# Performance work log

Hardware: AMD Instinct MI355X
Metric: run time of the kernel (lower is better)

## Reference

```python
import jax, jax.numpy as jnp
import numpy as np

N_NODES = 100000


def _sage_conv(x, src, dst, Wl, Wr, b):
    # PyG SAGEConv (aggr='mean'): out = lin_l(mean_j x_j) + lin_r(x_i)
    deg = jax.ops.segment_sum(jnp.ones_like(src, dtype=x.dtype), dst, num_segments=N_NODES)
    agg = jax.ops.segment_sum(x[src], dst, num_segments=N_NODES)
    agg = agg / jnp.clip(deg, 1.0)[:, None]
    return agg @ Wl.T + x @ Wr.T + b


def setup_inputs() -> dict:
    key = jax.random.key(0)
    ks = jax.random.split(key, 16)
    N, E, ES = N_NODES, 1600000, 100000
    IN, H, D = 64, 128, 64

    def lin(k, out_c, in_c):
        s = 1.0 / np.sqrt(in_c)
        return jax.random.uniform(k, (out_c, in_c), jnp.float32, -s, s)

    inp = {
        "x": jax.random.normal(ks[0], (N, IN), jnp.float32),
        "edge_index": jax.random.randint(ks[1], (2, E), 0, N, jnp.int64),
        "edge_sample": jax.random.randint(ks[2], (2, ES), 0, N, jnp.int64),
        # SAGEConv 0: 64 -> 128
        "Wl0": lin(ks[3], H, IN), "Wr0": lin(ks[4], H, IN), "b0": jnp.zeros((H,), jnp.float32),
        # SAGEConv 1: 128 -> 128
        "Wl1": lin(ks[5], H, H), "Wr1": lin(ks[6], H, H), "b1": jnp.zeros((H,), jnp.float32),
        # SAGEConv 2: 128 -> 64
        "Wl2": lin(ks[7], D, H), "Wr2": lin(ks[8], D, H), "b2": jnp.zeros((D,), jnp.float32),
        # feature decoder MLP: 64 -> 128 -> 64
        "Wd1": lin(ks[9], H, D), "bd1": jnp.zeros((H,), jnp.float32),
        "Wd2": lin(ks[10], IN, H), "bd2": jnp.zeros((IN,), jnp.float32),
    }
    return inp


def reference(x, edge_index, edge_sample, Wl0, Wr0, b0, Wl1, Wr1, b1, Wl2, Wr2, b2, Wd1, bd1, Wd2, bd2):
    src, dst = edge_index[0], edge_index[1]
    # encoder (dropout = identity at inference)
    h = jax.nn.relu(_sage_conv(x, src, dst, Wl0, Wr0, b0))
    h = jax.nn.relu(_sage_conv(h, src, dst, Wl1, Wr1, b1))
    emb = _sage_conv(h, src, dst, Wl2, Wr2, b2)
    # feature decoder
    rec = jax.nn.relu(emb @ Wd1.T + bd1) @ Wd2.T + bd2
    # edge decoder: dot product
    edge_scores = jnp.sum(emb[edge_sample[0]] * emb[edge_sample[1]], axis=1)
    return emb, rec, edge_scores
```

## Files before the change

### kernel.cpp

```cpp
#include <hip/hip_runtime.h>

#define NN 100000
#define NBK 196
#define CHUNK 8192
typedef unsigned int uint;
typedef unsigned short ushort;

using f32x4 = __attribute__((ext_vector_type(4))) float;
using s16x8 = __attribute__((ext_vector_type(8))) short;

__device__ inline ushort f32_to_bf16(float f) {
  uint u = __float_as_uint(f);
  uint r = (u + 0x7FFFu + ((u >> 16) & 1u)) >> 16;
  return (ushort)r;
}
__device__ inline float bf16_to_f32(ushort h) {
  return __uint_as_float(((uint)h) << 16);
}

typedef __attribute__((address_space(1))) const unsigned int gas_u32;
typedef __attribute__((address_space(3))) unsigned int las_u32;
__device__ __forceinline__ void gld_lds16(const void* gp, void* lp) {
  __builtin_amdgcn_global_load_lds((gas_u32*)gp, (las_u32*)lp, 16, 0, 0);
}

struct P8 { const float* p[8]; };

__global__ void k_prep(const int* __restrict__ dst, uint* __restrict__ bcnt,
                       uint* __restrict__ chunkCnt, int E, int NCB,
                       const float* __restrict__ x, ushort* __restrict__ xb, int n4, int NC,
                       P8 w, ushort* __restrict__ whi, int wtotal) {
  int b = blockIdx.x;
  int tid = threadIdx.x;
  if (b < NCB) {
    __shared__ uint hist[NBK];
    for (int i = tid; i < NBK; i += 256) hist[i] = 0;
    __syncthreads();
    int base = b * CHUNK;
    int lim = min(base + CHUNK, E);
    for (int e = base + tid; e < lim; e += 256) atomicAdd(&hist[(uint)dst[e] >> 9], 1u);
    __syncthreads();
    for (int i = tid; i < NBK; i += 256) {
      uint h = hist[i];
      chunkCnt[(i << 8) + b] = h;
      if (h) atomicAdd(&bcnt[i], h);
    }
  } else if (b < NCB + NC) {
    int i = (b - NCB) * 256 + tid;
    if (i < n4) {
      float4 v = ((const float4*)x)[i];
      uint2 o;
      o.x = (uint)f32_to_bf16(v.x) | ((uint)f32_to_bf16(v.y) << 16);
      o.y = (uint)f32_to_bf16(v.z) | ((uint)f32_to_bf16(v.w) << 16);
      ((uint2*)xb)[i] = o;
    }
  } else {
    int g = (b - NCB - NC) * 256 + tid;
    if (g < wtotal) {
      const int offs[8] = {0, 8192, 16384, 32768, 49152, 57344, 65536, 73728};
      int s = 0;
#pragma unroll
      for (int i = 1; i < 8; ++i) s += (g >= offs[i]);
      whi[g] = f32_to_bf16(w.p[s][g - offs[s]]);
    }
  }
}

__global__ void k_bscan(const uint* __restrict__ bcnt, uint* __restrict__ bbase,
                        int* __restrict__ rp, const uint* __restrict__ chunkCnt,
                        uint* __restrict__ chunkBase, int NCB) {
  int bk = blockIdx.x;
  int l = threadIdx.x;
  uint p = 0, tot = 0;
  for (int i = l; i < NBK; i += 64) {
    uint v = bcnt[i];
    tot += v;
    if (i < bk) p += v;
  }
#pragma unroll
  for (int off = 1; off < 64; off <<= 1) {
    p += __shfl_xor(p, off, 64);
    tot += __shfl_xor(tot, off, 64);
  }
  if (l == 0) {
    bbase[bk] = p;
    if (bk == 0) { bbase[NBK] = tot; rp[NN] = (int)tot; }
  }
  uint carry = p;
#pragma unroll
  for (int seg = 0; seg < 4; ++seg) {
    int c = seg * 64 + l;
    uint v = (c < NCB) ? chunkCnt[(bk << 8) + c] : 0u;
    uint incl = v;
#pragma unroll
    for (int off = 1; off < 64; off <<= 1) {
      uint t = __shfl_up(incl, off, 64);
      if (l >= off) incl += t;
    }
    if (c < NCB) chunkBase[(bk << 8) + c] = carry + incl - v;
    carry += __shfl(incl, 63, 64);
  }
}

__global__ void k_bscatter(const int* __restrict__ src, const int* __restrict__ dst,
                           const uint* __restrict__ chunkBase, uint* __restrict__ packed, int E) {
  __shared__ uint cur[NBK];
  int tid = threadIdx.x;
  int b = blockIdx.x;
  for (int i = tid; i < NBK; i += 256) cur[i] = chunkBase[(i << 8) + b];
  __syncthreads();
  int base = b * CHUNK;
  int lim = min(base + CHUNK, E);
  for (int e = base + tid; e < lim; e += 256) {
    uint d = (uint)dst[e];
    uint s = (uint)src[e];
    uint bk = d >> 9;
    uint p = atomicAdd(&cur[bk], 1u);
    packed[p] = ((d & 511u) << 20) | s;
  }
}

__global__ void k_build(const uint* __restrict__ bbase, const uint* __restrict__ packed,
                        int* __restrict__ rp, int* __restrict__ col) {
  __shared__ uint hist[512];
  __shared__ uint ws[256];
  int b = blockIdx.x;
  int tid = threadIdx.x;
  uint lo = bbase[b], hi = bbase[b + 1];
  hist[tid] = 0;
  hist[tid + 256] = 0;
  __syncthreads();
  for (uint e = lo + tid; e < hi; e += 256) atomicAdd(&hist[packed[e] >> 20], 1u);
  __syncthreads();
  uint v0 = hist[tid * 2], v1 = hist[tid * 2 + 1];
  ws[tid] = v0 + v1;
  __syncthreads();
  for (int off = 1; off < 256; off <<= 1) {
    uint add = (tid >= off) ? ws[tid - off] : 0u;
    __syncthreads();
    ws[tid] += add;
    __syncthreads();
  }
  uint ex = (tid > 0) ? ws[tid - 1] : 0u;
  hist[tid * 2] = ex;
  hist[tid * 2 + 1] = ex + v0;
  int nodeBase = b << 9;
#pragma unroll
  for (int i = 0; i < 2; ++i) {
    int node = nodeBase + tid * 2 + i;
    if (node < NN) rp[node] = (int)(lo + hist[tid * 2 + i]);
  }
  __syncthreads();
  for (uint e = lo + tid; e < hi; e += 256) {
    uint pk = packed[e];
    uint p = atomicAdd(&hist[pk >> 20], 1u);
    col[lo + p] = (int)(pk & 0xFFFFFu);
  }
}

#define ACC1(vv) { alo += __uint_as_float((vv) << 16); ahi += __uint_as_float((vv) & 0xffff0000u); }

template <int F, int MODE>
__global__ void k_agg(const ushort* __restrict__ x, const int* __restrict__ rp,
                      const int* __restrict__ col, const ushort* __restrict__ u,
                      float* __restrict__ of, ushort* __restrict__ ob, int n) {
  constexpr int RS = F / 2;
  int wave = (blockIdx.x * blockDim.x + threadIdx.x) >> 6;
  int lane = threadIdx.x & 63;
  int node, l;
  if (F == 128) { node = wave; l = lane; }
  else { node = wave * 2 + (lane >> 5); l = lane & 31; }
  if (node >= n) return;
  int beg = rp[node], end = rp[node + 1];
  int deg = end - beg;
  const uint* __restrict__ xu = (const uint*)x;
  float alo = 0.f, ahi = 0.f;
  int j = beg;
  for (; j + 8 <= end; j += 8) {
    int c0 = col[j], c1 = col[j + 1], c2 = col[j + 2], c3 = col[j + 3];
    int c4 = col[j + 4], c5 = col[j + 5], c6 = col[j + 6], c7 = col[j + 7];
    uint v0 = xu[(size_t)c0 * RS + l];
    uint v1 = xu[(size_t)c1 * RS + l];
    uint v2 = xu[(size_t)c2 * RS + l];
    uint v3 = xu[(size_t)c3 * RS + l];
    uint v4 = xu[(size_t)c4 * RS + l];
    uint v5 = xu[(size_t)c5 * RS + l];
    uint v6 = xu[(size_t)c6 * RS + l];
    uint v7 = xu[(size_t)c7 * RS + l];
    ACC1(v0) ACC1(v1) ACC1(v2) ACC1(v3) ACC1(v4) ACC1(v5) ACC1(v6) ACC1(v7)
  }
  if (j + 4 <= end) {
    int c0 = col[j], c1 = col[j + 1], c2 = col[j + 2], c3 = col[j + 3];
    uint v0 = xu[(size_t)c0 * RS + l];
    uint v1 = xu[(size_t)c1 * RS + l];
    uint v2 = xu[(size_t)c2 * RS + l];
    uint v3 = xu[(size_t)c3 * RS + l];
    ACC1(v0) ACC1(v1) ACC1(v2) ACC1(v3)
    j += 4;
  }
  for (; j < end; ++j) {
    uint v0 = xu[(size_t)col[j] * RS + l];
    ACC1(v0)
  }
  float inv = 1.0f / (float)(deg > 0 ? deg : 1);
  alo *= inv;
  ahi *= inv;
  if (MODE == 0) {
    ((uint*)ob)[(size_t)node * RS + l] = (uint)f32_to_bf16(alo) | ((uint)f32_to_bf16(ahi) << 16);
  } else {
    uint uv = ((const uint*)u)[(size_t)node * RS + l];
    float e0 = alo + __uint_as_float(uv << 16);
    float e1 = ahi + __uint_as_float(uv & 0xffff0000u);
    ((float2*)of)[(size_t)node * RS + l] = make_float2(e0, e1);
    ((uint*)ob)[(size_t)node * RS + l] = (uint)f32_to_bf16(e0) | ((uint)f32_to_bf16(e1) << 16);
  }
}

template <int K, bool RELU, bool DUAL, int OUTM>
__global__ __launch_bounds__(256) void k_gemm(
    const ushort* __restrict__ A, const ushort* __restrict__ Wa,
    const ushort* __restrict__ B, const ushort* __restrict__ Wb,
    const float* __restrict__ bias,
    ushort* __restrict__ outu, ushort* __restrict__ outb, int n) {
  constexpr int BM = 64;
  constexpr int KT = 32;
  constexpr int TPP = K / KT;
  constexpr int T = (DUAL ? 2 : 1) * TPP;
  __shared__ ushort As[2][BM * KT];
  __shared__ ushort Ws[2][128 * KT];

  const int tid = threadIdx.x;
  const int lane = tid & 63;
  const int wid = tid >> 6;
  const int fr = lane & 15;
  const int fq = lane >> 4;
  const int blockRow = blockIdx.x * BM;
  const int rowBase = (wid >> 1) * 32;
  const int colBase = (wid & 1) * 64;
  const int srow = lane >> 2;
  const int sksrc = (lane & 3) ^ ((lane >> 3) & 3);
  const bool fullTile = (blockRow + BM <= n);

  f32x4 acc[2][4];
#pragma unroll
  for (int mi = 0; mi < 2; ++mi)
#pragma unroll
    for (int ni = 0; ni < 4; ++ni) acc[mi][ni] = (f32x4){0.f, 0.f, 0.f, 0.f};

  auto stage = [&](int buf, int t) {
    const ushort* __restrict__ Ap = (DUAL && t >= TPP) ? B : A;
    const ushort* __restrict__ Wp = (DUAL && t >= TPP) ? Wb : Wa;
    const int ktb = (t % TPP) * KT;
    {
      int r0 = wid * 16;
      gld_lds16(Ap + (size_t)(blockRow + r0 + srow) * K + ktb + sksrc * 8,
                (char*)As[buf] + r0 * 64);
    }
#pragma unroll
    for (int i = 0; i < 2; ++i) {
      int r0 = (wid + i * 4) * 16;
      gld_lds16(Wp + (size_t)(r0 + srow) * K + ktb + sksrc * 8,
                (char*)Ws[buf] + r0 * 64);
    }
  };
  auto compute = [&](int buf) {
    s16x8 af[2], wf[4];
#pragma unroll
    for (int mi = 0; mi < 2; ++mi) {
      int r = rowBase + mi * 16 + fr;
      af[mi] = *(const s16x8*)((const char*)As[buf] + r * 64 + ((fq ^ ((r >> 1) & 3)) << 4));
    }
#pragma unroll
    for (int ni = 0; ni < 4; ++ni) {
      int r = colBase + ni * 16 + fr;
      wf[ni] = *(const s16x8*)((const char*)Ws[buf] + r * 64 + ((fq ^ ((r >> 1) & 3)) << 4));
    }
#pragma unroll
    for (int mi = 0; mi < 2; ++mi)
#pragma unroll
      for (int ni = 0; ni < 4; ++ni)
        acc[mi][ni] = __builtin_amdgcn_mfma_f32_16x16x32_bf16(af[mi], wf[ni], acc[mi][ni], 0, 0, 0);
  };

  if (fullTile) {
    stage(0, 0);
#pragma unroll
    for (int t = 0; t < T; ++t) {
      if (t + 1 < T) {
        stage((t + 1) & 1, t + 1);
        asm volatile("s_waitcnt vmcnt(3)" ::: "memory");
      } else {
        asm volatile("s_waitcnt vmcnt(0)" ::: "memory");
      }
      __builtin_amdgcn_sched_barrier(0);
      __builtin_amdgcn_s_barrier();
      compute(t & 1);
      if (t + 1 < T) __builtin_amdgcn_s_barrier();
    }
  } else {
#pragma unroll
    for (int t = 0; t < T; ++t) {
      const ushort* __restrict__ Ap = (DUAL && t >= TPP) ? B : A;
      const ushort* __restrict__ Wp = (DUAL && t >= TPP) ? Wb : Wa;
      const int ktb = (t % TPP) * KT;
      __syncthreads();
      {
        int c = tid;
        int r = c >> 2, s = c & 3;
        int row = blockRow + r;
        int ds = s ^ ((r >> 1) & 3);
        uint4 v = make_uint4(0u, 0u, 0u, 0u);
        if (row < n) v = *(const uint4*)(Ap + (size_t)row * K + ktb + s * 8);
        *(uint4*)((char*)As[0] + r * 64 + (ds << 4)) = v;
      }
      for (int c = tid; c < 128 * 4; c += 256) {
        int r = c >> 2, s = c & 3;
        int ds = s ^ ((r >> 1) & 3);
        *(uint4*)((char*)Ws[0] + r * 64 + (ds << 4)) =
            *(const uint4*)(Wp + (size_t)r * K + ktb + s * 8);
      }
      __syncthreads();
      compute(0);
    }
  }

#pragma unroll
  for (int mi = 0; mi < 2; ++mi) {
#pragma unroll
    for (int ni = 0; ni < 4; ++ni) {
#pragma unroll
      for (int r = 0; r < 4; ++r) {
        int row = blockRow + rowBase + mi * 16 + fq * 4 + r;
        int colI = colBase + ni * 16 + fr;
        if (row < n) {
          float v = acc[mi][ni][r];
          if (OUTM == 3) {
            if (colI < 64)
              outb[(size_t)row * 64 + colI] = f32_to_bf16(v);
            else
              outu[(size_t)row * 64 + (colI - 64)] = f32_to_bf16(v + bias[colI - 64]);
          } else {
            if (bias) v += bias[colI];
            if (RELU) v = fmaxf(v, 0.f);
            outb[(size_t)row * 128 + colI] = f32_to_bf16(v);
          }
        }
      }
    }
  }
}

__global__ __launch_bounds__(256) void k_dec(
    const ushort* __restrict__ emb, const ushort* __restrict__ Wd1,
    const float* __restrict__ bd1, const ushort* __restrict__ Wd2,
    const float* __restrict__ bd2, float* __restrict__ rec, int n) {
  __shared__ ushort smem[24 * 1024];
  ushort* As = smem;
  ushort* W1 = smem + 8192;
  ushort* W2 = smem + 16384;
  ushort* Hs = smem;

  const int tid = threadIdx.x;
  const int lane = tid & 63;
  const int wid = tid >> 6;
  const int fr = lane & 15;
  const int fq = lane >> 4;
  const int blockRow = blockIdx.x * 128;
  const int rowBase1 = (wid >> 1) * 64;
  const int colBase1 = (wid & 1) * 64;
  const int srow8 = lane >> 3, sl8 = lane & 7;
  const int srow4 = lane >> 4, sl16 = lane & 15;
  const bool fullTile = (blockRow + 128 <= n);

  if (fullTile) {
#pragma unroll
    for (int i = 0; i < 4; ++i) {
      int r0 = (wid + i * 4) * 8;
      gld_lds16(emb + (size_t)(blockRow + r0 + srow8) * 64 + (sl8 ^ srow8) * 8,
                (char*)As + r0 * 128);
    }
#pragma unroll
    for (int i = 0; i < 4; ++i) {
      int r0 = (wid + i * 4) * 8;
      gld_lds16(Wd1 + (size_t)(r0 + srow8) * 64 + (sl8 ^ srow8) * 8, (char*)W1 + r0 * 128);
    }
#pragma unroll
    for (int i = 0; i < 4; ++i) {
      int r0 = (wid + i * 4) * 4;
      int grow = r0 + srow4;
      gld_lds16(Wd2 + (size_t)grow * 128 + (sl16 ^ (grow & 7)) * 8, (char*)W2 + r0 * 256);
    }
  } else {
    for (int c = tid; c < 128 * 8; c += 256) {
      int r = c >> 3, s = c & 7;
      int row = blockRow + r;
      uint4 v = make_uint4(0u, 0u, 0u, 0u);
      if (row < n) v = *(const uint4*)(emb + (size_t)row * 64 + s * 8);
      *(uint4*)((char*)As + r * 128 + ((s ^ (r & 7)) << 4)) = v;
    }
    for (int c = tid; c < 128 * 8; c += 256) {
      int r = c >> 3, s = c & 7;
      *(uint4*)((char*)W1 + r * 128 + ((s ^ (r & 7)) << 4)) =
          *(const uint4*)(Wd1 + (size_t)r * 64 + s * 8);
    }
    for (int c = tid; c < 64 * 16; c += 256) {
      int r = c >> 4, s = c & 15;
      *(uint4*)((char*)W2 + r * 256 + ((s ^ (r & 7)) << 4)) =
          *(const uint4*)(Wd2 + (size_t)r * 128 + s * 8);
    }
  }
  __syncthreads();

  f32x4 a1[4][4];
#pragma unroll
  for (int mi = 0; mi < 4; ++mi)
#pragma unroll
    for (int ni = 0; ni < 4; ++ni) a1[mi][ni] = (f32x4){0.f, 0.f, 0.f, 0.f};
#pragma unroll
  for (int ks = 0; ks < 2; ++ks) {
    s16x8 af[4], wf[4];
#pragma unroll
    for (int mi = 0; mi < 4; ++mi) {
      int r = rowBase1 + mi * 16 + fr;
      af[mi] = *(const s16x8*)((const char*)As + r * 128 + (((ks * 4 + fq) ^ (r & 7)) << 4));
    }
#pragma unroll
    for (int ni = 0; ni < 4; ++ni) {
      int r = colBase1 + ni * 16 + fr;
      wf[ni] = *(const s16x8*)((const char*)W1 + r * 128 + (((ks * 4 + fq) ^ (r & 7)) << 4));
    }
#pragma unroll
    for (int mi = 0; mi < 4; ++mi)
#pragma unroll
      for (int ni = 0; ni < 4; ++ni)
        a1[mi][ni] = __builtin_amdgcn_mfma_f32_16x16x32_bf16(af[mi], wf[ni], a1[mi][ni], 0, 0, 0);
  }
  __syncthreads();
#pragma unroll
  for (int mi = 0; mi < 4; ++mi) {
#pragma unroll
    for (int ni = 0; ni < 4; ++ni) {
#pragma unroll
      for (int r = 0; r < 4; ++r) {
        int rowl = rowBase1 + mi * 16 + fq * 4 + r;
        int colI = colBase1 + ni * 16 + fr;
        float v = fmaxf(a1[mi][ni][r] + bd1[colI], 0.f);
        int byte = rowl * 256 + ((((colI >> 3) ^ (rowl & 7))) << 4) + (colI & 7) * 2;
        *(ushort*)((char*)Hs + byte) = f32_to_bf16(v);
      }
    }
  }
  __syncthreads();

  f32x4 a2[2][4];
#pragma unroll
  for (int mi = 0; mi < 2; ++mi)
#pragma unroll
    for (int ni = 0; ni < 4; ++ni) a2[mi][ni] = (f32x4){0.f, 0.f, 0.f, 0.f};
#pragma unroll
  for (int kk = 0; kk < 4; ++kk) {
    s16x8 af[2], wf[4];
#pragma unroll
    for (int mi = 0; mi < 2; ++mi) {
      int r = wid * 32 + mi * 16 + fr;
      af[mi] = *(const s16x8*)((const char*)Hs + r * 256 + (((kk * 4 + fq) ^ (r & 7)) << 4));
    }
#pragma unroll
    for (int ni = 0; ni < 4; ++ni) {
      int r = ni * 16 + fr;
      wf[ni] = *(const s16x8*)((const char*)W2 + r * 256 + (((kk * 4 + fq) ^ (r & 7)) << 4));
    }
#pragma unroll
    for (int mi = 0; mi < 2; ++mi)
#pragma unroll
      for (int ni = 0; ni < 4; ++ni)
        a2[mi][ni] = __builtin_amdgcn_mfma_f32_16x16x32_bf16(af[mi], wf[ni], a2[mi][ni], 0, 0, 0);
  }
#pragma unroll
  for (int mi = 0; mi < 2; ++mi) {
#pragma unroll
    for (int ni = 0; ni < 4; ++ni) {
#pragma unroll
      for (int r = 0; r < 4; ++r) {
        int row = blockRow + wid * 32 + mi * 16 + fq * 4 + r;
        int colI = ni * 16 + fr;
        if (row < n) rec[(size_t)row * 64 + colI] = a2[mi][ni][r] + bd2[colI];
      }
    }
  }
}

__global__ void k_dot(const float* __restrict__ emb, const int* __restrict__ ea,
                      const int* __restrict__ eb, float* __restrict__ out, int ne) {
  int hw = (blockIdx.x * blockDim.x + threadIdx.x) >> 5;
  int l = threadIdx.x & 31;
  if (hw >= ne) return;
  float2 a = ((const float2*)(emb + (size_t)ea[hw] * 64))[l];
  float2 b = ((const float2*)(emb + (size_t)eb[hw] * 64))[l];
  float v = a.x * b.x + a.y * b.y;
#pragma unroll
  for (int off = 16; off; off >>= 1) v += __shfl_xor(v, off, 64);
  if (l == 0) out[hw] = v;
}

extern "C" void kernel_launch(void* const* d_in, const int* in_sizes, int n_in,
                              void* d_out, int out_size, void* d_ws, size_t ws_size,
                              hipStream_t stream) {
  const float* x = (const float*)d_in[0];
  const int* ei = (const int*)d_in[1];
  const int* es = (const int*)d_in[2];
  const float* b0 = (const float*)d_in[5];
  const float* b1 = (const float*)d_in[8];
  const float* b2 = (const float*)d_in[11];
  const float* bd1 = (const float*)d_in[13];
  const float* bd2 = (const float*)d_in[15];

  const int E = in_sizes[1] / 2;
  const int ES = in_sizes[2] / 2;
  const int* srcv = ei;
  const int* dstv = ei + E;
  const int* ea = es;
  const int* eb = es + ES;

  char* wp = (char*)d_ws;
  auto alloc = [&](size_t bytes) {
    char* p = wp;
    wp += (bytes + 511) & ~(size_t)511;
    return p;
  };
  int* row_ptr = (int*)alloc((NN + 1) * sizeof(int));
  uint* bcnt = (uint*)alloc(NBK * sizeof(uint));
  uint* bbase = (uint*)alloc((NBK + 1) * sizeof(uint));
  uint* chunkCnt = (uint*)alloc((size_t)NBK * 256 * sizeof(uint));
  uint* chunkBase = (uint*)alloc((size_t)NBK * 256 * sizeof(uint));
  uint* packed = (uint*)alloc((size_t)E * sizeof(uint));
  int* colv = (int*)alloc((size_t)E * sizeof(int));
  ushort* xb = (ushort*)alloc((size_t)NN * 64 * 2);
  ushort* aggb = (ushort*)alloc((size_t)NN * 128 * 2);
  ushort* h1b = (ushort*)alloc((size_t)NN * 128 * 2);
  ushort* h2b = (ushort*)alloc((size_t)NN * 128 * 2);
  ushort* ub = (ushort*)alloc((size_t)NN * 64 * 2);
  ushort* embb = (ushort*)alloc((size_t)NN * 64 * 2);
  ushort* Whb = (ushort*)alloc(81920 * 2);

  const int WO0 = 0, WO1 = 8192, WO2 = 16384, WO3 = 32768, WO4 = 49152,
            WO6 = 65536, WO7 = 73728;

  float* out_emb = (float*)d_out;
  float* out_rec = out_emb + (size_t)NN * 64;
  float* out_sc = out_rec + (size_t)NN * 64;

  hipMemsetAsync(bcnt, 0, NBK * sizeof(uint), stream);

  P8 wptrs;
  wptrs.p[0] = (const float*)d_in[3];  wptrs.p[1] = (const float*)d_in[4];
  wptrs.p[2] = (const float*)d_in[6];  wptrs.p[3] = (const float*)d_in[7];
  wptrs.p[4] = (const float*)d_in[9];  wptrs.p[5] = (const float*)d_in[10];
  wptrs.p[6] = (const float*)d_in[12]; wptrs.p[7] = (const float*)d_in[14];

  const int NCB = (E + CHUNK - 1) / CHUNK;
  const int n4 = NN * 64 / 4;
  const int NC = (n4 + 255) / 256;
  const int NS = (81920 + 255) / 256;
  k_prep<<<NCB + NC + NS, 256, 0, stream>>>(dstv, bcnt, chunkCnt, E, NCB, x, xb, n4, NC,
                                            wptrs, Whb, 81920);
  k_bscan<<<NBK, 64, 0, stream>>>(bcnt, bbase, row_ptr, chunkCnt, chunkBase, NCB);
  k_bscatter<<<NCB, 256, 0, stream>>>(srcv, dstv, chunkBase, packed, E);
  k_build<<<NBK, 256, 0, stream>>>(bbase, packed, row_ptr, colv);

  const int g64 = (NN + 7) / 8;
  const int g128a = (NN + 3) / 4;
  dim3 gg((NN + 63) / 64);

  k_agg<64, 0><<<g64, 256, 0, stream>>>(xb, row_ptr, colv, nullptr, nullptr, aggb, NN);
  k_gemm<64, true, true, 0><<<gg, 256, 0, stream>>>(
      aggb, Whb + WO0, xb, Whb + WO1, b0, nullptr, h1b, NN);
  k_agg<128, 0><<<g128a, 256, 0, stream>>>(h1b, row_ptr, colv, nullptr, nullptr, aggb, NN);
  k_gemm<128, true, true, 0><<<gg, 256, 0, stream>>>(
      aggb, Whb + WO2, h1b, Whb + WO3, b1, nullptr, h2b, NN);
  k_gemm<128, false, false, 3><<<gg, 256, 0, stream>>>(
      h2b, Whb + WO4, nullptr, nullptr, b2, ub, aggb, NN);
  k_agg<64, 2><<<g64, 256, 0, stream>>>(aggb, row_ptr, colv, ub, out_emb, embb, NN);
  k_dec<<<(NN + 127) / 128, 256, 0, stream>>>(embb, Whb + WO6, bd1, Whb + WO7, bd2, out_rec, NN);
  k_dot<<<(ES + 7) / 8, 256, 0, stream>>>(out_emb, ea, eb, out_sc, ES);
}
```

Baseline: 297.6 us.

## Fuse neighbor aggregation into SAGE GEMMs and decoder kernels

Merges each mean-aggregation gather with the following dual GEMM (layers 0 and 1), and folds the final-layer aggregation into the feature decoder kernel. The aggregated rows and self features are written straight into shared memory, which removes the intermediate aggregate buffers and their global round trips and cuts kernel launches. Weights are now read from global memory directly into MFMA fragments instead of being staged in LDS. Gather parallelism per block is lower (64 or 128 nodes per block, looped serially), so latency hiding for the irregular gathers may suffer.

```diff
diff --git a/kernel.cpp b/kernel.cpp
--- a/kernel.cpp
+++ b/kernel.cpp
@@ -160,59 +160,224 @@
 
 #define ACC1(vv) { alo += __uint_as_float((vv) << 16); ahi += __uint_as_float((vv) & 0xffff0000u); }
 
-template <int F, int MODE>
-__global__ void k_agg(const ushort* __restrict__ x, const int* __restrict__ rp,
-                      const int* __restrict__ col, const ushort* __restrict__ u,
-                      float* __restrict__ of, ushort* __restrict__ ob, int n) {
-  constexpr int RS = F / 2;
-  int wave = (blockIdx.x * blockDim.x + threadIdx.x) >> 6;
-  int lane = threadIdx.x & 63;
-  int node, l;
-  if (F == 128) { node = wave; l = lane; }
-  else { node = wave * 2 + (lane >> 5); l = lane & 31; }
-  if (node >= n) return;
+__device__ __forceinline__ void gather64(const uint* __restrict__ xu, const int* __restrict__ rp,
+                                         const int* __restrict__ col, int node, int l,
+                                         float& alo, float& ahi) {
   int beg = rp[node], end = rp[node + 1];
   int deg = end - beg;
-  const uint* __restrict__ xu = (const uint*)x;
-  float alo = 0.f, ahi = 0.f;
+  alo = 0.f; ahi = 0.f;
   int j = beg;
   for (; j + 8 <= end; j += 8) {
     int c0 = col[j], c1 = col[j + 1], c2 = col[j + 2], c3 = col[j + 3];
     int c4 = col[j + 4], c5 = col[j + 5], c6 = col[j + 6], c7 = col[j + 7];
-    uint v0 = xu[(size_t)c0 * RS + l];
-    uint v1 = xu[(size_t)c1 * RS + l];
-    uint v2 = xu[(size_t)c2 * RS + l];
-    uint v3 = xu[(size_t)c3 * RS + l];
-    uint v4 = xu[(size_t)c4 * RS + l];
-    uint v5 = xu[(size_t)c5 * RS + l];
-    uint v6 = xu[(size_t)c6 * RS + l];
-    uint v7 = xu[(size_t)c7 * RS + l];
+    uint v0 = xu[(size_t)c0 * 32 + l];
+    uint v1 = xu[(size_t)c1 * 32 + l];
+    uint v2 = xu[(size_t)c2 * 32 + l];
+    uint v3 = xu[(size_t)c3 * 32 + l];
+    uint v4 = xu[(size_t)c4 * 32 + l];
+    uint v5 = xu[(size_t)c5 * 32 + l];
+    uint v6 = xu[(size_t)c6 * 32 + l];
+    uint v7 = xu[(size_t)c7 * 32 + l];
     ACC1(v0) ACC1(v1) ACC1(v2) ACC1(v3) ACC1(v4) ACC1(v5) ACC1(v6) ACC1(v7)
   }
   if (j + 4 <= end) {
     int c0 = col[j], c1 = col[j + 1], c2 = col[j + 2], c3 = col[j + 3];
-    uint v0 = xu[(size_t)c0 * RS + l];
-    uint v1 = xu[(size_t)c1 * RS + l];
-    uint v2 = xu[(size_t)c2 * RS + l];
-    uint v3 = xu[(size_t)c3 * RS + l];
+    uint v0 = xu[(size_t)c0 * 32 + l];
+    uint v1 = xu[(size_t)c1 * 32 + l];
+    uint v2 = xu[(size_t)c2 * 32 + l];
+    uint v3 = xu[(size_t)c3 * 32 + l];
     ACC1(v0) ACC1(v1) ACC1(v2) ACC1(v3)
     j += 4;
   }
   for (; j < end; ++j) {
-    uint v0 = xu[(size_t)col[j] * RS + l];
+    uint v0 = xu[(size_t)col[j] * 32 + l];
     ACC1(v0)
   }
   float inv = 1.0f / (float)(deg > 0 ? deg : 1);
   alo *= inv;
   ahi *= inv;
-  if (MODE == 0) {
-    ((uint*)ob)[(size_t)node * RS + l] = (uint)f32_to_bf16(alo) | ((uint)f32_to_bf16(ahi) << 16);
-  } else {
-    uint uv = ((const uint*)u)[(size_t)node * RS + l];
-    float e0 = alo + __uint_as_float(uv << 16);
-    float e1 = ahi + __uint_as_float(uv & 0xffff0000u);
-    ((float2*)of)[(size_t)node * RS + l] = make_float2(e0, e1);
-    ((uint*)ob)[(size_t)node * RS + l] = (uint)f32_to_bf16(e0) | ((uint)f32_to_bf16(e1) << 16);
+}
+
+__global__ __launch_bounds__(256) void k_fused64(
+    const ushort* __restrict__ xb, const int* __restrict__ rp, const int* __restrict__ col,
+    const ushort* __restrict__ Wl, const ushort* __restrict__ Wr,
+    const float* __restrict__ bias, ushort* __restrict__ out, int n) {
+  __shared__ ushort As[64 * 128];
+  const int tid = threadIdx.x;
+  const int lane = tid & 63;
+  const int wid = tid >> 6;
+  const int fr = lane & 15;
+  const int fq = lane >> 4;
+  const int blockRow = blockIdx.x * 64;
+  const int hw = tid >> 5;
+  const int l = tid & 31;
+  const uint* xu = (const uint*)xb;
+
+#pragma unroll 1
+  for (int it = 0; it < 8; ++it) {
+    int r = it * 8 + hw;
+    int node = blockRow + r;
+    uint pk_agg = 0u, pk_self = 0u;
+    if (node < n) {
+      float alo, ahi;
+      gather64(xu, rp, col, node, l, alo, ahi);
+      pk_agg = (uint)f32_to_bf16(alo) | ((uint)f32_to_bf16(ahi) << 16);
+      pk_self = xu[(size_t)node * 32 + l];
+    }
+    int sa = (l >> 2) ^ (r & 7);
+    int ss = (8 + (l >> 2)) ^ (r & 7);
+    *(uint*)((char*)As + r * 256 + (sa << 4) + (l & 3) * 4) = pk_agg;
+    *(uint*)((char*)As + r * 256 + (ss << 4) + (l & 3) * 4) = pk_self;
+  }
+  __syncthreads();
+
+  const int rowBase = (wid >> 1) * 32;
+  const int colBase = (wid & 1) * 64;
+  f32x4 acc[2][4];
+#pragma unroll
+  for (int mi = 0; mi < 2; ++mi)
+#pragma unroll
+    for (int ni = 0; ni < 4; ++ni) acc[mi][ni] = (f32x4){0.f, 0.f, 0.f, 0.f};
+#pragma unroll
+  for (int ks = 0; ks < 4; ++ks) {
+    s16x8 af[2], wf[4];
+#pragma unroll
+    for (int mi = 0; mi < 2; ++mi) {
+      int r = rowBase + mi * 16 + fr;
+      af[mi] = *(const s16x8*)((const char*)As + r * 256 + (((ks * 4 + fq) ^ (r & 7)) << 4));
+    }
+#pragma unroll
+    for (int ni = 0; ni < 4; ++ni) {
+      int r2 = colBase + ni * 16 + fr;
+      const ushort* wp = (ks < 2) ? (Wl + (size_t)r2 * 64 + ks * 32 + fq * 8)
+                                  : (Wr + (size_t)r2 * 64 + (ks - 2) * 32 + fq * 8);
+      wf[ni] = *(const s16x8*)wp;
+    }
+#pragma unroll
+    for (int mi = 0; mi < 2; ++mi)
+#pragma unroll
+      for (int ni = 0; ni < 4; ++ni)
+        acc[mi][ni] = __builtin_amdgcn_mfma_f32_16x16x32_bf16(af[mi], wf[ni], acc[mi][ni], 0, 0, 0);
+  }
+#pragma unroll
+  for (int mi = 0; mi < 2; ++mi) {
+#pragma unroll
+    for (int ni = 0; ni < 4; ++ni) {
+#pragma unroll
+      for (int r = 0; r < 4; ++r) {
+        int row = blockRow + rowBase + mi * 16 + fq * 4 + r;
+        int colI = colBase + ni * 16 + fr;
+        if (row < n) {
+          float v = fmaxf(acc[mi][ni][r] + bias[colI], 0.f);
+          out[(size_t)row * 128 + colI] = f32_to_bf16(v);
+        }
+      }
+    }
+  }
+}
+
+__global__ __launch_bounds__(256) void k_fused128(
+    const ushort* __restrict__ hb, const int* __restrict__ rp, const int* __restrict__ col,
+    const ushort* __restrict__ Wl, const ushort* __restrict__ Wr,
+    const float* __restrict__ bias, ushort* __restrict__ out, int n) {
+  __shared__ ushort As[64 * 256];
+  const int tid = threadIdx.x;
+  const int lane = tid & 63;
+  const int wid = tid >> 6;
+  const int fr = lane & 15;
+  const int fq = lane >> 4;
+  const int blockRow = blockIdx.x * 64;
+  const uint* xu = (const uint*)hb;
+
+#pragma unroll 1
+  for (int it = 0; it < 16; ++it) {
+    int r = it * 4 + wid;
+    int node = blockRow + r;
+    uint pk_agg = 0u, pk_self = 0u;
+    if (node < n) {
+      int beg = rp[node], end = rp[node + 1];
+      int deg = end - beg;
+      float alo = 0.f, ahi = 0.f;
+      int j = beg;
+      for (; j + 8 <= end; j += 8) {
+        int c0 = col[j], c1 = col[j + 1], c2 = col[j + 2], c3 = col[j + 3];
+        int c4 = col[j + 4], c5 = col[j + 5], c6 = col[j + 6], c7 = col[j + 7];
+        uint v0 = xu[(size_t)c0 * 64 + lane];
+        uint v1 = xu[(size_t)c1 * 64 + lane];
+        uint v2 = xu[(size_t)c2 * 64 + lane];
+        uint v3 = xu[(size_t)c3 * 64 + lane];
+        uint v4 = xu[(size_t)c4 * 64 + lane];
+        uint v5 = xu[(size_t)c5 * 64 + lane];
+        uint v6 = xu[(size_t)c6 * 64 + lane];
+        uint v7 = xu[(size_t)c7 * 64 + lane];
+        ACC1(v0) ACC1(v1) ACC1(v2) ACC1(v3) ACC1(v4) ACC1(v5) ACC1(v6) ACC1(v7)
+      }
+      if (j + 4 <= end) {
+        int c0 = col[j], c1 = col[j + 1], c2 = col[j + 2], c3 = col[j + 3];
+        uint v0 = xu[(size_t)c0 * 64 + lane];
+        uint v1 = xu[(size_t)c1 * 64 + lane];
+        uint v2 = xu[(size_t)c2 * 64 + lane];
+        uint v3 = xu[(size_t)c3 * 64 + lane];
+        ACC1(v0) ACC1(v1) ACC1(v2) ACC1(v3)
+        j += 4;
+      }
+      for (; j < end; ++j) {
+        uint v0 = xu[(size_t)col[j] * 64 + lane];
+        ACC1(v0)
+      }
+      float inv = 1.0f / (float)(deg > 0 ? deg : 1);
+      pk_agg = (uint)f32_to_bf16(alo * inv) | ((uint)f32_to_bf16(ahi * inv) << 16);
+      pk_self = xu[(size_t)node * 64 + lane];
+    }
+    int sa = (lane >> 2) ^ (r & 7);
+    int ss = (16 + (lane >> 2)) ^ (r & 7);
+    *(uint*)((char*)As + r * 512 + (sa << 4) + (lane & 3) * 4) = pk_agg;
+    *(uint*)((char*)As + r * 512 + (ss << 4) + (lane & 3) * 4) = pk_self;
+  }
+  __syncthreads();
+
+  const int rowBase = (wid >> 1) * 32;
+  const int colBase = (wid & 1) * 64;
+  f32x4 acc[2][4];
+#pragma unroll
+  for (int mi = 0; mi < 2; ++mi)
+#pragma unroll
+    for (int ni = 0; ni < 4; ++ni) acc[mi][ni] = (f32x4){0.f, 0.f, 0.f, 0.f};
+#pragma unroll
+  for (int ks = 0; ks < 8; ++ks) {
+    s16x8 af[2], wf[4];
+#pragma unroll
+    for (int mi = 0; mi < 2; ++mi) {
+      int r = rowBase + mi * 16 + fr;
+      af[mi] = *(const s16x8*)((const char*)As + r * 512 + (((ks * 4 + fq) ^ (r & 7)) << 4));
+    }
+#pragma unroll
+    for (int ni = 0; ni < 4; ++ni) {
+      int r2 = colBase + ni * 16 + fr;
+      const ushort* wp = (ks < 4) ? (Wl + (size_t)r2 * 128 + ks * 32 + fq * 8)
+                                  : (Wr + (size_t)r2 * 128 + (ks - 4) * 32 + fq * 8);
+      wf[ni] = *(const s16x8*)wp;
+    }
+#pragma unroll
+    for (int mi = 0; mi < 2; ++mi)
+#pragma unroll
+      for (int ni = 0; ni < 4; ++ni)
+        acc[mi][ni] = __builtin_amdgcn_mfma_f32_16x16x32_bf16(af[mi], wf[ni], acc[mi][ni], 0, 0, 0);
+  }
+#pragma unroll
+  for (int mi = 0; mi < 2; ++mi) {
+#pragma unroll
+    for (int ni = 0; ni < 4; ++ni) {
+#pragma unroll
+      for (int r = 0; r < 4; ++r) {
+        int row = blockRow + rowBase + mi * 16 + fq * 4 + r;
+        int colI = colBase + ni * 16 + fr;
+        if (row < n) {
+          float v = fmaxf(acc[mi][ni][r] + bias[colI], 0.f);
+          out[(size_t)row * 128 + colI] = f32_to_bf16(v);
+        }
+      }
+    }
   }
 }
 
@@ -350,10 +515,12 @@
   }
 }
 
-__global__ __launch_bounds__(256) void k_dec(
-    const ushort* __restrict__ emb, const ushort* __restrict__ Wd1,
-    const float* __restrict__ bd1, const ushort* __restrict__ Wd2,
-    const float* __restrict__ bd2, float* __restrict__ rec, int n) {
+__global__ __launch_bounds__(256) void k_aggdec(
+    const ushort* __restrict__ tb, const int* __restrict__ rp, const int* __restrict__ col,
+    const ushort* __restrict__ ub, float* __restrict__ out_emb,
+    const ushort* __restrict__ Wd1, const float* __restrict__ bd1,
+    const ushort* __restrict__ Wd2, const float* __restrict__ bd2,
+    float* __restrict__ rec, int n) {
   __shared__ ushort smem[24 * 1024];
   ushort* As = smem;
   ushort* W1 = smem + 8192;
@@ -366,51 +533,46 @@
   const int fr = lane & 15;
   const int fq = lane >> 4;
   const int blockRow = blockIdx.x * 128;
+  const int hw = tid >> 5;
+  const int l = tid & 31;
+  const int srow8 = lane >> 3, sl8 = lane & 7;
+  const int srow4 = lane >> 4, sl16 = lane & 15;
+  const uint* tu = (const uint*)tb;
+  const uint* uu = (const uint*)ub;
+
+#pragma unroll
+  for (int i = 0; i < 4; ++i) {
+    int r0 = (wid + i * 4) * 8;
+    gld_lds16(Wd1 + (size_t)(r0 + srow8) * 64 + (sl8 ^ srow8) * 8, (char*)W1 + r0 * 128);
+  }
+#pragma unroll
+  for (int i = 0; i < 4; ++i) {
+    int r0 = (wid + i * 4) * 4;
+    int grow = r0 + srow4;
+    gld_lds16(Wd2 + (size_t)grow * 128 + (sl16 ^ (grow & 7)) * 8, (char*)W2 + r0 * 256);
+  }
+
+#pragma unroll 1
+  for (int it = 0; it < 16; ++it) {
+    int r = it * 8 + hw;
+    int node = blockRow + r;
+    uint pk = 0u;
+    if (node < n) {
+      float alo, ahi;
+      gather64(tu, rp, col, node, l, alo, ahi);
+      uint uv = uu[(size_t)node * 32 + l];
+      float e0 = alo + __uint_as_float(uv << 16);
+      float e1 = ahi + __uint_as_float(uv & 0xffff0000u);
+      ((float2*)out_emb)[(size_t)node * 32 + l] = make_float2(e0, e1);
+      pk = (uint)f32_to_bf16(e0) | ((uint)f32_to_bf16(e1) << 16);
+    }
+    int sa = (l >> 2) ^ (r & 7);
+    *(uint*)((char*)As + r * 128 + (sa << 4) + (l & 3) * 4) = pk;
+  }
+  __syncthreads();
+
   const int rowBase1 = (wid >> 1) * 64;
   const int colBase1 = (wid & 1) * 64;
-  const int srow8 = lane >> 3, sl8 = lane & 7;
-  const int srow4 = lane >> 4, sl16 = lane & 15;
-  const bool fullTile = (blockRow + 128 <= n);
-
-  if (fullTile) {
-#pragma unroll
-    for (int i = 0; i < 4; ++i) {
-      int r0 = (wid + i * 4) * 8;
-      gld_lds16(emb + (size_t)(blockRow + r0 + srow8) * 64 + (sl8 ^ srow8) * 8,
-                (char*)As + r0 * 128);
-    }
-#pragma unroll
-    for (int i = 0; i < 4; ++i) {
-      int r0 = (wid + i * 4) * 8;
-      gld_lds16(Wd1 + (size_t)(r0 + srow8) * 64 + (sl8 ^ srow8) * 8, (char*)W1 + r0 * 128);
-    }
-#pragma unroll
-    for (int i = 0; i < 4; ++i) {
-      int r0 = (wid + i * 4) * 4;
-      int grow = r0 + srow4;
-      gld_lds16(Wd2 + (size_t)grow * 128 + (sl16 ^ (grow & 7)) * 8, (char*)W2 + r0 * 256);
-    }
-  } else {
-    for (int c = tid; c < 128 * 8; c += 256) {
-      int r = c >> 3, s = c & 7;
-      int row = blockRow + r;
-      uint4 v = make_uint4(0u, 0u, 0u, 0u);
-      if (row < n) v = *(const uint4*)(emb + (size_t)row * 64 + s * 8);
-      *(uint4*)((char*)As + r * 128 + ((s ^ (r & 7)) << 4)) = v;
-    }
-    for (int c = tid; c < 128 * 8; c += 256) {
-      int r = c >> 3, s = c & 7;
-      *(uint4*)((char*)W1 + r * 128 + ((s ^ (r & 7)) << 4)) =
-          *(const uint4*)(Wd1 + (size_t)r * 64 + s * 8);
-    }
-    for (int c = tid; c < 64 * 16; c += 256) {
-      int r = c >> 4, s = c & 15;
-      *(uint4*)((char*)W2 + r * 256 + ((s ^ (r & 7)) << 4)) =
-          *(const uint4*)(Wd2 + (size_t)r * 128 + s * 8);
-    }
-  }
-  __syncthreads();
-
   f32x4 a1[4][4];
 #pragma unroll
   for (int mi = 0; mi < 4; ++mi)
@@ -536,11 +698,10 @@
   uint* packed = (uint*)alloc((size_t)E * sizeof(uint));
   int* colv = (int*)alloc((size_t)E * sizeof(int));
   ushort* xb = (ushort*)alloc((size_t)NN * 64 * 2);
-  ushort* aggb = (ushort*)alloc((size_t)NN * 128 * 2);
+  ushort* tbuf = (ushort*)alloc((size_t)NN * 64 * 2);
   ushort* h1b = (ushort*)alloc((size_t)NN * 128 * 2);
   ushort* h2b = (ushort*)alloc((size_t)NN * 128 * 2);
   ushort* ub = (ushort*)alloc((size_t)NN * 64 * 2);
-  ushort* embb = (ushort*)alloc((size_t)NN * 64 * 2);
   ushort* Whb = (ushort*)alloc(81920 * 2);
 
   const int WO0 = 0, WO1 = 8192, WO2 = 16384, WO3 = 32768, WO4 = 49152,
@@ -568,19 +729,13 @@
   k_bscatter<<<NCB, 256, 0, stream>>>(srcv, dstv, chunkBase, packed, E);
   k_build<<<NBK, 256, 0, stream>>>(bbase, packed, row_ptr, colv);
 
-  const int g64 = (NN + 7) / 8;
-  const int g128a = (NN + 3) / 4;
   dim3 gg((NN + 63) / 64);
 
-  k_agg<64, 0><<<g64, 256, 0, stream>>>(xb, row_ptr, colv, nullptr, nullptr, aggb, NN);
-  k_gemm<64, true, true, 0><<<gg, 256, 0, stream>>>(
-      aggb, Whb + WO0, xb, Whb + WO1, b0, nullptr, h1b, NN);
-  k_agg<128, 0><<<g128a, 256, 0, stream>>>(h1b, row_ptr, colv, nullptr, nullptr, aggb, NN);
-  k_gemm<128, true, true, 0><<<gg, 256, 0, stream>>>(
-      aggb, Whb + WO2, h1b, Whb + WO3, b1, nullptr, h2b, NN);
+  k_fused64<<<gg, 256, 0, stream>>>(xb, row_ptr, colv, Whb + WO0, Whb + WO1, b0, h1b, NN);
+  k_fused128<<<gg, 256, 0, stream>>>(h1b, row_ptr, colv, Whb + WO2, Whb + WO3, b1, h2b, NN);
   k_gemm<128, false, false, 3><<<gg, 256, 0, stream>>>(
-      h2b, Whb + WO4, nullptr, nullptr, b2, ub, aggb, NN);
-  k_agg<64, 2><<<g64, 256, 0, stream>>>(aggb, row_ptr, colv, ub, out_emb, embb, NN);
-  k_dec<<<(NN + 127) / 128, 256, 0, stream>>>(embb, Whb + WO6, bd1, Whb + WO7, bd2, out_rec, NN);
+      h2b, Whb + WO4, nullptr, nullptr, b2, ub, tbuf, NN);
+  k_aggdec<<<(NN + 127) / 128, 256, 0, stream>>>(
+      tbuf, row_ptr, colv, ub, out_emb, Whb + WO6, bd1, Whb + WO7, bd2, out_rec, NN);
   k_dot<<<(ES + 7) / 8, 256, 0, stream>>>(out_emb, ea, eb, out_sc, ES);
 }
```

After: 450.6 us. 51.4% more time.
